# Kernel optimization log

Measured on AMD Instinct MI355X. Metric: run time of the kernel, lower is better.

## Reference

```python
import jax, jax.numpy as jnp
import numpy as np

N = 2048  # num_nodes (perfect binary tree, heap on nodes 1..N-1, root = node 1)
B = 2048  # batch of independent (phase1, phase2) pairs


def _build_tree(n):
    # left[j]/right[j] hold the compliance SLOT of node j's heap children (2j, 2j+1).
    # Slot of node j is n - j (body loop writes compliance[:, i] at step i with j = n - i).
    left = -np.ones(n, dtype=np.int32)
    right = -np.ones(n, dtype=np.int32)
    for j in range(1, n // 2):
        left[j] = n - 2 * j
        right[j] = n - (2 * j + 1)
    return jnp.array(left), jnp.array(right)


def setup_inputs() -> dict:
    key = jax.random.key(0)
    k1, k2, k3, k4, k5, k6, k7 = jax.random.split(key, 7)

    def make_phase(kd, ko):
        # SPD-ish compliance vectors [d0, o0, o1, d1, o2, d2]: diag in [1,2], off-diag small
        diag = 1.0 + jax.random.uniform(kd, (B, 3))
        off = 0.2 * (jax.random.uniform(ko, (B, 3)) - 0.5)
        return jnp.stack([diag[:, 0], off[:, 0], off[:, 1], diag[:, 1], off[:, 2], diag[:, 2]], axis=-1)

    phase1 = make_phase(k1, k2)
    phase2 = make_phase(k3, k4)
    theta = 0.5 * jax.random.normal(k5, (N,), dtype=jnp.float32)
    activation = jax.random.normal(k6, (N,), dtype=jnp.float32)
    weight = jnp.zeros((N,), dtype=jnp.float32)
    fractions = 0.05 + jax.random.uniform(k7, (N,), dtype=jnp.float32)
    left, right = _build_tree(N)
    return {"phase1": phase1, "phase2": phase2, "theta": theta, "activation": activation,
            "weight": weight, "fractions": fractions, "left": left, "right": right}


def _rot(theta):
    c = jnp.cos(theta)
    s = jnp.sin(theta)
    r2 = jnp.sqrt(jnp.asarray(2.0, theta.dtype))
    return jnp.array([[c * c, s * s, r2 * c * s],
                      [s * s, c * c, -r2 * c * s],
                      [-r2 * s * c, r2 * s * c, c * c - s * s]])


def _rotate_b(v, theta):
    # v: [B,6] Mandel vector -> [B,3,3] -> R(-t) @ M @ R(t) -> [B,6]
    M = jnp.stack([
        jnp.stack([v[:, 0], v[:, 1], v[:, 2]], -1),
        jnp.stack([v[:, 1], v[:, 3], v[:, 4]], -1),
        jnp.stack([v[:, 2], v[:, 4], v[:, 5]], -1)], -2)
    Rm = _rot(theta)
    Rn = _rot(-theta)
    D = jnp.einsum('ij,bjk,kl->bil', Rn, M, Rm)
    return jnp.stack([D[:, 0, 0], D[:, 0, 1], D[:, 0, 2], D[:, 1, 1], D[:, 1, 2], D[:, 2, 2]], -1)


def _homogenise_b(D1, D2, f1, f2):
    # D1, D2: [B,6]; f1, f2 scalars
    gamma = f1 * D2[:, 0] + f2 * D1[:, 0]
    g = jnp.where(gamma == 0, 1.0, gamma)  # guard: only hits discarded leaf-step lanes
    ff = f1 * f2 / g
    d0 = D1[:, 0] * D2[:, 0] / g
    d1 = (f1 * D1[:, 1] * D2[:, 0] + f2 * D2[:, 1] * D1[:, 0]) / g
    d2 = (f1 * D1[:, 2] * D2[:, 0] + f2 * D2[:, 2] * D1[:, 0]) / g
    d3 = f1 * D1[:, 3] + f2 * D2[:, 3] - ff * (D1[:, 1] - D2[:, 1]) ** 2
    d4 = f1 * D1[:, 4] + f2 * D2[:, 4] - ff * (D1[:, 2] - D2[:, 2]) * (D1[:, 1] - D2[:, 1])
    d5 = f1 * D1[:, 5] + f2 * D2[:, 5] - ff * (D1[:, 2] - D2[:, 2]) ** 2
    return jnp.stack([d0, d1, d2, d3, d4, d5], -1)


def _forward(phase1, phase2, theta, fractions, left, right):
    n = theta.shape[0]
    b = phase1.shape[0]

    def step(compliance, i):
        j = n - i                      # node processed at step i (original clamps OOB gathers)
        jj = jnp.minimum(j, n - 1)     # emulate jax's OOB-index clamping at j == n
        l = left[jj]
        r = right[jj]
        is_leaf = (l == -1) & (r == -1)
        # jnp dynamic indexing wraps negative indices: -1 -> n-1
        lw = jnp.where(l < 0, l + n, l)
        rw = jnp.where(r < 0, r + n, r)
        D1 = compliance[:, lw]
        D2 = compliance[:, rw]
        Dh = _homogenise_b(D1, D2, fractions[lw], fractions[rw])
        base = jnp.where((j % 2) == 0, phase1, phase2)  # leaf parity uses unclamped j
        val = jnp.where(is_leaf, base, Dh)
        out = _rotate_b(val, theta[jj])
        return compliance.at[:, i].set(out), None

    compliance = jnp.zeros((b, n, 6), dtype=phase1.dtype)
    compliance, _ = jax.lax.scan(step, compliance, jnp.arange(n))
    return compliance[:, -1]


def reference(phase1, phase2, theta, activation, weight, fractions, left, right):
    n = theta.shape[0]

    # Faithful replication of the original's weight/fraction propagation loops.
    # Note: as in the source, body_fun reads self.fractions (not the propagated fs),
    # so these loops do NOT affect the output (dead code, DCE'd under jit).
    def prop_w(i, ws):
        j = jnp.minimum(n - i, n - 1)
        l = left[j]
        r = right[j]
        is_leaf = (l == -1) & (r == -1)
        upd = jnp.where(is_leaf, jnp.maximum(activation[j], 0.0), ws[l] + ws[r])
        return ws.at[j].set(upd)

    ws = jax.lax.fori_loop(0, n + 1, prop_w, weight)

    def prop_f(i, fs):
        j = jnp.minimum(n - i, n - 1)
        l = left[j]
        r = right[j]
        is_leaf = (l == -1) & (r == -1)
        upd = jnp.where(is_leaf, 0.0, ws[l] / ws[j])
        fs = fs.at[l].set(upd)
        return fs.at[r].set(upd)

    _fs = jax.lax.fori_loop(5, n + 1, prop_f, fractions)  # unused, matching the source

    return _forward(phase1, phase2, theta, fractions, left, right)
```

## Files before the change

kernel.cpp:

```cpp
#include <hip/hip_runtime.h>


#define N_NODES 2048

__device__ __forceinline__ void rotate6(const float* m, float4 r, float* o) {
    float a = r.x, bb = r.y, d = r.z, e = r.w;
    float T00 = m[0]*a  + m[1]*bb - m[2]*d;
    float T01 = m[0]*bb + m[1]*a  + m[2]*d;
    float T02 = (m[0]-m[1])*d + m[2]*e;
    float T10 = m[1]*a  + m[3]*bb - m[4]*d;
    float T11 = m[1]*bb + m[3]*a  + m[4]*d;
    float T12 = (m[1]-m[3])*d + m[4]*e;
    float T20 = m[2]*a  + m[4]*bb - m[5]*d;
    float T21 = m[2]*bb + m[4]*a  + m[5]*d;
    float T22 = (m[2]-m[4])*d + m[5]*e;
    o[0] = a*T00 + bb*T10 - d*T20;
    o[1] = a*T01 + bb*T11 - d*T21;
    o[2] = a*T02 + bb*T12 - d*T22;
    o[3] = bb*T01 + a*T11 + d*T21;
    o[4] = bb*T02 + a*T12 + d*T22;
    o[5] = (T02 - T12)*d + e*T22;
}

__device__ __forceinline__ void homog6(const float* D1, const float* D2,
                                       float f1, float f2, float* o) {
    float gamma = f1*D2[0] + f2*D1[0];
    float g = (gamma == 0.0f) ? 1.0f : gamma;
    float rg = 1.0f / g;
    float ff = f1*f2*rg;
    o[0] = D1[0]*D2[0]*rg;
    o[1] = (f1*D1[1]*D2[0] + f2*D2[1]*D1[0])*rg;
    o[2] = (f1*D1[2]*D2[0] + f2*D2[2]*D1[0])*rg;
    float t1 = D1[1]-D2[1];
    float t2 = D1[2]-D2[2];
    o[3] = f1*D1[3] + f2*D2[3] - ff*t1*t1;
    o[4] = f1*D1[4] + f2*D2[4] - ff*t2*t1;
    o[5] = f1*D1[5] + f2*D2[5] - ff*t2*t2;
}

__device__ __forceinline__ void subtree9(const float* p1, const float* p2,
                                         const float4* __restrict__ rot,
                                         const float2* __restrict__ fr,
                                         int j9, float* outD) {
    float L[6], R[6], H[6];
    rotate6(p1, rot[2*j9],   L);
    rotate6(p2, rot[2*j9+1], R);
    float2 f = fr[j9];
    homog6(L, R, f.x, f.y, H);
    rotate6(H, rot[j9], outD);
}

__global__ void setup_kernel(const float* __restrict__ theta,
                             const float* __restrict__ fractions,
                             float4* __restrict__ rot, float2* __restrict__ fr) {
    int j = blockIdx.x * blockDim.x + threadIdx.x;
    if (j >= 1 && j < N_NODES) {
        float t = theta[j];
        float c = cosf(t), s = sinf(t);
        float a = c*c, bb = s*s;
        float d = sqrtf(2.0f) * c * s;
        rot[j] = make_float4(a, bb, d, a - bb);
    }
    if (j >= 1 && j < N_NODES/2) {
        fr[j] = make_float2(fractions[N_NODES - 2*j], fractions[N_NODES - 2*j - 1]);
    }
}

__global__ __launch_bounds__(256) void tree_kernel(
    const float* __restrict__ phase1, const float* __restrict__ phase2,
    const float4* __restrict__ rot, const float2* __restrict__ fr,
    float* __restrict__ out)
{
    __shared__ float V[6][512];
    const int b = blockIdx.x;
    const int tid = threadIdx.x;

    float p1[6], p2[6];
#pragma unroll
    for (int k = 0; k < 6; ++k) { p1[k] = phase1[b*6+k]; p2[k] = phase2[b*6+k]; }

    {
        int j8 = 256 + tid;
        float DA[6], DB[6], Dh[6], Dn[6];
        subtree9(p1, p2, rot, fr, 2*j8,   DA);
        subtree9(p1, p2, rot, fr, 2*j8+1, DB);
        float2 f = fr[j8];
        homog6(DA, DB, f.x, f.y, Dh);
        rotate6(Dh, rot[j8], Dn);
#pragma unroll
        for (int k = 0; k < 6; ++k) V[k][j8] = Dn[k];
    }
    __syncthreads();

#pragma unroll 1
    for (int Lw = 128; Lw >= 2; Lw >>= 1) {
        if (tid < Lw) {
            int j = Lw + tid;
            float D1[6], D2[6], Dh[6], Dn[6];
#pragma unroll
            for (int k = 0; k < 6; ++k) {
                float2 ch = ((const float2*)&V[k][0])[j];
                D1[k] = ch.x; D2[k] = ch.y;
            }
            float2 f = fr[j];
            homog6(D1, D2, f.x, f.y, Dh);
            rotate6(Dh, rot[j], Dn);
#pragma unroll
            for (int k = 0; k < 6; ++k) V[k][j] = Dn[k];
        }
        __syncthreads();
    }

    if (tid == 0) {
        float D1[6], D2[6], Dh[6], Dn[6];
#pragma unroll
        for (int k = 0; k < 6; ++k) {
            float2 ch = ((const float2*)&V[k][0])[1];
            D1[k] = ch.x; D2[k] = ch.y;
        }
        float2 f = fr[1];
        homog6(D1, D2, f.x, f.y, Dh);
        rotate6(Dh, rot[1], Dn);
#pragma unroll
        for (int k = 0; k < 6; ++k) out[b*6 + k] = Dn[k];
    }
}

extern "C" void kernel_launch(void* const* d_in, const int* in_sizes, int n_in,
                              void* d_out, int out_size, void* d_ws, size_t ws_size,
                              hipStream_t stream) {
    const float* phase1    = (const float*)d_in[0];
    const float* phase2    = (const float*)d_in[1];
    const float* theta     = (const float*)d_in[2];
    const float* fractions = (const float*)d_in[5];
    float* out = (float*)d_out;

    const int B = in_sizes[0] / 6;

    float4* rot = (float4*)d_ws;
    float2* fr  = (float2*)((char*)d_ws + N_NODES * sizeof(float4));

    hipLaunchKernelGGL(setup_kernel, dim3((N_NODES + 255) / 256), dim3(256), 0, stream,
                       theta, fractions, rot, fr);
    hipLaunchKernelGGL(tree_kernel, dim3(B), dim3(256), 0, stream,
                       phase1, phase2, rot, fr, out);
}
```

Before: 78.36 us.

## Reduce tree with wave shuffles, two batch items per block, 128 threads each

```diff
diff --git a/kernel.cpp b/kernel.cpp
--- a/kernel.cpp
+++ b/kernel.cpp
@@ -50,6 +50,18 @@
     rotate6(H, rot[j9], outD);
 }
 
+__device__ __forceinline__ void node8(const float* p1, const float* p2,
+                                      const float4* __restrict__ rot,
+                                      const float2* __restrict__ fr,
+                                      int j8, float* outD) {
+    float A[6], B[6], H[6];
+    subtree9(p1, p2, rot, fr, 2*j8,   A);
+    subtree9(p1, p2, rot, fr, 2*j8+1, B);
+    float2 f = fr[j8];
+    homog6(A, B, f.x, f.y, H);
+    rotate6(H, rot[j8], outD);
+}
+
 __global__ void setup_kernel(const float* __restrict__ theta,
                              const float* __restrict__ fractions,
                              float4* __restrict__ rot, float2* __restrict__ fr) {
@@ -66,63 +78,69 @@
     }
 }
 
-__global__ __launch_bounds__(256) void tree_kernel(
+__global__ __launch_bounds__(256, 4) void tree_kernel(
     const float* __restrict__ phase1, const float* __restrict__ phase2,
     const float4* __restrict__ rot, const float2* __restrict__ fr,
     float* __restrict__ out)
 {
-    __shared__ float V[6][512];
-    const int b = blockIdx.x;
-    const int tid = threadIdx.x;
+    const int tid  = threadIdx.x;
+    const int wid  = tid >> 6;
+    const int lane = tid & 63;
+    const int half = wid & 1;
+    const int bloc = wid >> 1;
+    const int b    = blockIdx.x * 2 + bloc;
 
     float p1[6], p2[6];
 #pragma unroll
     for (int k = 0; k < 6; ++k) { p1[k] = phase1[b*6+k]; p2[k] = phase2[b*6+k]; }
 
+    float A[6], Bv[6], H[6], v[6];
     {
-        int j8 = 256 + tid;
-        float DA[6], DB[6], Dh[6], Dn[6];
-        subtree9(p1, p2, rot, fr, 2*j8,   DA);
-        subtree9(p1, p2, rot, fr, 2*j8+1, DB);
-        float2 f = fr[j8];
-        homog6(DA, DB, f.x, f.y, Dh);
-        rotate6(Dh, rot[j8], Dn);
+        int j7 = 128 + half*64 + lane;
+        node8(p1, p2, rot, fr, 2*j7,   A);
+        node8(p1, p2, rot, fr, 2*j7+1, Bv);
+        float2 f = fr[j7];
+        homog6(A, Bv, f.x, f.y, H);
+        rotate6(H, rot[j7], v);
+    }
+
+    int jbase = 128 + half*64;
+    int width = 64;
 #pragma unroll
-        for (int k = 0; k < 6; ++k) V[k][j8] = Dn[k];
+    for (int s = 0; s < 6; ++s) {
+        float ce[6], co[6];
+#pragma unroll
+        for (int k = 0; k < 6; ++k) {
+            ce[k] = __shfl(v[k], 2*lane,     64);
+            co[k] = __shfl(v[k], 2*lane + 1, 64);
+        }
+        jbase >>= 1;
+        width >>= 1;
+        if (lane < width) {
+            int j = jbase + lane;
+            float2 f = fr[j];
+            homog6(ce, co, f.x, f.y, H);
+            rotate6(H, rot[j], v);
+        }
+    }
+
+    __shared__ float comb[2][2][6];
+    if (lane == 0) {
+#pragma unroll
+        for (int k = 0; k < 6; ++k) comb[bloc][half][k] = v[k];
     }
     __syncthreads();
 
-#pragma unroll 1
-    for (int Lw = 128; Lw >= 2; Lw >>= 1) {
-        if (tid < Lw) {
-            int j = Lw + tid;
-            float D1[6], D2[6], Dh[6], Dn[6];
+    if (tid < 2) {
+        float D1[6], D2[6], Hh[6], Dn[6];
 #pragma unroll
-            for (int k = 0; k < 6; ++k) {
-                float2 ch = ((const float2*)&V[k][0])[j];
-                D1[k] = ch.x; D2[k] = ch.y;
-            }
-            float2 f = fr[j];
-            homog6(D1, D2, f.x, f.y, Dh);
-            rotate6(Dh, rot[j], Dn);
+        for (int k = 0; k < 6; ++k) { D1[k] = comb[tid][0][k]; D2[k] = comb[tid][1][k]; }
+        float2 f = fr[1];
+        homog6(D1, D2, f.x, f.y, Hh);
+        rotate6(Hh, rot[1], Dn);
+        int bb = blockIdx.x * 2 + tid;
 #pragma unroll
-            for (int k = 0; k < 6; ++k) V[k][j] = Dn[k];
-        }
-        __syncthreads();
-    }
-
-    if (tid == 0) {
-        float D1[6], D2[6], Dh[6], Dn[6];
-#pragma unroll
-        for (int k = 0; k < 6; ++k) {
-            float2 ch = ((const float2*)&V[k][0])[1];
-            D1[k] = ch.x; D2[k] = ch.y;
-        }
-        float2 f = fr[1];
-        homog6(D1, D2, f.x, f.y, Dh);
-        rotate6(Dh, rot[1], Dn);
-#pragma unroll
-        for (int k = 0; k < 6; ++k) out[b*6 + k] = Dn[k];
+        for (int k = 0; k < 6; ++k) out[bb*6 + k] = Dn[k];
     }
 }
 
@@ -142,6 +160,6 @@
 
     hipLaunchKernelGGL(setup_kernel, dim3((N_NODES + 255) / 256), dim3(256), 0, stream,
                        theta, fractions, rot, fr);
-    hipLaunchKernelGGL(tree_kernel, dim3(B), dim3(256), 0, stream,
+    hipLaunchKernelGGL(tree_kernel, dim3(B / 2), dim3(256), 0, stream,
                        phase1, phase2, rot, fr, out);
 }
```

Measured after the change: 83.53 us. 6.6% more time.
